# Kernel tuning notes

Hardware: AMD Instinct MI355X
Metric: run time of the kernel (lower is better)

The kernel has to match this reference:

```python
import jax, jax.numpy as jnp
import numpy as np

N_ATOMS = 100000
N_PAIRS = 3200000
F_ATOM, F_PAIR, H, F_OUT = 75, 14, 50, 50


def _linear_params(key, fan_in, fan_out):
    # torch.nn.Linear default init: U(-1/sqrt(fan_in), 1/sqrt(fan_in))
    kw, kb = jax.random.split(key)
    bound = 1.0 / np.sqrt(fan_in)
    W = jax.random.uniform(kw, (fan_out, fan_in), jnp.float32, -bound, bound)
    b = jax.random.uniform(kb, (fan_out,), jnp.float32, -bound, bound)
    return W, b


def setup_inputs() -> dict:
    key = jax.random.key(0)
    ks = jax.random.split(key, 12)
    atom_features = jax.random.normal(ks[0], (N_ATOMS, F_ATOM), jnp.float32)
    pair_features = jax.random.normal(ks[1], (N_PAIRS, F_PAIR), jnp.float32)
    pair_split = jnp.sort(jax.random.randint(ks[2], (N_PAIRS,), 0, N_ATOMS, jnp.int32))
    atom_to_pair = jax.random.randint(ks[3], (N_PAIRS, 2), 0, N_ATOMS, jnp.int32)
    W_AA, b_AA = _linear_params(ks[4], F_ATOM, H)
    W_PA, b_PA = _linear_params(ks[5], F_PAIR, H)
    W_A, b_A = _linear_params(ks[6], 2 * H, F_OUT)
    W_AP, b_AP = _linear_params(ks[7], 2 * F_ATOM, H)
    W_PP, b_PP = _linear_params(ks[8], F_PAIR, H)
    W_P, b_P = _linear_params(ks[9], 2 * H, F_OUT)
    return dict(atom_features=atom_features, pair_features=pair_features,
                pair_split=pair_split, atom_to_pair=atom_to_pair,
                W_AA=W_AA, b_AA=b_AA, W_PA=W_PA, b_PA=b_PA,
                W_A=W_A, b_A=b_A, W_AP=W_AP, b_AP=b_AP,
                W_PP=W_PP, b_PP=b_PP, W_P=W_P, b_P=b_P)


def reference(atom_features, pair_features, pair_split, atom_to_pair,
              W_AA, b_AA, W_PA, b_PA, W_A, b_A,
              W_AP, b_AP, W_PP, b_PP, W_P, b_P):
    relu = jax.nn.relu
    # atom update
    AA = relu(atom_features @ W_AA.T + b_AA)                      # [N_atoms, H]
    PA = relu(pair_features @ W_PA.T + b_PA)                      # [N_pairs, H]
    PA = jax.ops.segment_sum(PA, pair_split, num_segments=N_ATOMS)  # [N_atoms, H]
    A = relu(jnp.concatenate([AA, PA], axis=1) @ W_A.T + b_A)     # [N_atoms, F_OUT]
    # pair update
    pair_ij = atom_features[atom_to_pair].reshape(-1, 2 * F_ATOM)             # [N_pairs, 2F]
    pair_ji = atom_features[atom_to_pair[:, ::-1]].reshape(-1, 2 * F_ATOM)    # flipped order
    AP_ij = relu(pair_ij @ W_AP.T + b_AP)
    AP_ji = relu(pair_ji @ W_AP.T + b_AP)
    PP = relu(pair_features @ W_PP.T + b_PP)
    P = relu(jnp.concatenate([AP_ij + AP_ji, PP], axis=1) @ W_P.T + b_P)      # [N_pairs, F_OUT]
    return A, P
```

## Files before the change

kernel.cpp:

```cpp
#include <hip/hip_runtime.h>

#define NATOMS 100000
#define NPAIRS 3200000

using short8  = __attribute__((ext_vector_type(8))) short;
using float4v = __attribute__((ext_vector_type(4))) float;
using fx2     = __attribute__((ext_vector_type(2))) float;

__device__ __forceinline__ unsigned short f2bf(float f) {
    unsigned int u = __float_as_uint(f);
    unsigned int r = (u + 0x7fffu + ((u >> 16) & 1u)) >> 16;
    return (unsigned short)r;
}
__device__ __forceinline__ float bflo(unsigned int u) { return __uint_as_float(u << 16); }
__device__ __forceinline__ float bfhi(unsigned int u) { return __uint_as_float(u & 0xffff0000u); }
__device__ __forceinline__ unsigned int cvtpk(float lo, float hi) {
    unsigned int r;
    asm("v_cvt_pk_bf16_f32 %0, %1, %2" : "=v"(r) : "v"(lo), "v"(hi));
    return r;
}

__device__ __forceinline__ unsigned int fp8e(float v) {
    unsigned int u = __float_as_uint(v);
    unsigned int a = u & 0x7fffffffu;
    unsigned int r = a + 0x7FFFFu + ((a >> 20) & 1u);
    int e8 = (int)(r >> 23) - 120;
    unsigned int b = (e8 >= 1) ? (((unsigned int)e8 << 3) | ((r >> 20) & 7u)) : 0u;
    return b | ((u >> 24) & 0x80u);
}

#if __has_builtin(__builtin_amdgcn_cvt_pk_fp8_f32)
__device__ __forceinline__ unsigned int enc4(float a, float b, float c, float d) {
    int w = __builtin_amdgcn_cvt_pk_fp8_f32(a, b, 0, false);
    w = __builtin_amdgcn_cvt_pk_fp8_f32(c, d, w, true);
    return (unsigned int)w;
}
__device__ __forceinline__ unsigned short enc2(float a, float b) {
    return (unsigned short)(__builtin_amdgcn_cvt_pk_fp8_f32(a, b, 0, false) & 0xffff);
}
#else
__device__ __forceinline__ unsigned int enc4(float a, float b, float c, float d) {
    return fp8e(a) | (fp8e(b) << 8) | (fp8e(c) << 16) | (fp8e(d) << 24);
}
__device__ __forceinline__ unsigned short enc2(float a, float b) {
    return (unsigned short)(fp8e(a) | (fp8e(b) << 8));
}
#endif

#if __has_builtin(__builtin_amdgcn_cvt_pk_f32_fp8)
__device__ __forceinline__ fx2 dec8lo(unsigned int u) { return __builtin_amdgcn_cvt_pk_f32_fp8((int)u, false); }
__device__ __forceinline__ fx2 dec8hi(unsigned int u) { return __builtin_amdgcn_cvt_pk_f32_fp8((int)u, true); }
#else
__device__ __forceinline__ float fp8d_(unsigned int u, int sh) {
    unsigned int b = (u >> sh) & 0xffu;
    return __uint_as_float((((b & 0x7fu) << 20) + 0x3C000000u) | ((b & 0x80u) << 24));
}
__device__ __forceinline__ fx2 dec8lo(unsigned int u) { fx2 r; r.x = fp8d_(u, 0);  r.y = fp8d_(u, 8);  return r; }
__device__ __forceinline__ fx2 dec8hi(unsigned int u) { fx2 r; r.x = fp8d_(u, 16); r.y = fp8d_(u, 24); return r; }
#endif


__global__ __launch_bounds__(256) void k_wconv(
    const float* __restrict__ W_P,  const float* __restrict__ b_P,
    const float* __restrict__ W_PP, const float* __restrict__ b_PP,
    const float* __restrict__ W_PA, const float* __restrict__ b_PA,
    const float* __restrict__ W_AA, const float* __restrict__ b_AA,
    const float* __restrict__ W_AP, const float* __restrict__ b_AP,
    const float* __restrict__ W_A,  const float* __restrict__ b_A,
    unsigned short* __restrict__ WPb,  unsigned short* __restrict__ WPPb,
    unsigned short* __restrict__ WPAb, unsigned short* __restrict__ WATb,
    unsigned short* __restrict__ WAb,  float* __restrict__ PAsum)
{
    const int idx = blockIdx.x * 256 + threadIdx.x;
    if (idx < 64 * 128) {
        const int n = idx >> 7, k = idx & 127;
        float v = 0.0f, va = 0.0f;
        if (n < 50) {
            if (k < 50)                  { v = W_P[n * 100 + k];            va = W_A[n * 100 + k]; }
            else if (k == 50)            { v = b_P[n];                      va = b_A[n]; }
            else if (k >= 52 && k < 102) { v = W_P[n * 100 + 50 + (k - 52)]; va = W_A[n * 100 + 50 + (k - 52)]; }
        }
        WPb[idx] = f2bf(v);
        WAb[idx] = f2bf(va);
    }
    if (idx < 64 * 32) {
        const int n = idx >> 5, k = idx & 31;
        float vp = 0.0f, va = 0.0f;
        if (n < 50) {
            if (k < 14)      { vp = W_PP[n * 14 + k]; va = W_PA[n * 14 + k]; }
            else if (k == 14){ vp = b_PP[n];          va = b_PA[n]; }
        }
        WPPb[idx] = f2bf(vp);
        WPAb[idx] = f2bf(va);
    }
    if (idx < 160 * 96) {
        const int n = idx / 96, k = idx - n * 96;
        float v = 0.0f;
        if (n < 50) {
            if (k < 75)       v = W_AA[n * 75 + k];
            else if (k == 75) v = b_AA[n];
        } else if (n >= 52 && n < 102) {
            if (k < 75)       v = W_AP[(n - 52) * 150 + k];
            else if (k == 75) v = b_AP[n - 52];
        } else if (n >= 104 && n < 154) {
            if (k < 75)       v = W_AP[(n - 104) * 150 + 75 + k];
        }
        WATb[idx] = f2bf(v);
    }
    for (int i = idx; i < NATOMS * 50; i += 256 * 256) PAsum[i] = 0.0f;
}

__global__ __launch_bounds__(512) void k_atom_pre(
    const float* __restrict__ af,
    const unsigned short* __restrict__ WATb,
    unsigned short* __restrict__ AAb,
    unsigned short* __restrict__ XAu16)
{
    __shared__ unsigned short U16[128 * 128];

    const int t   = threadIdx.x;
    const int blk = blockIdx.x;
    const int pl  = t >> 2;
    const int sub = t & 3;
    const int w   = t >> 6;
    const int l   = t & 63;
    const int lr  = l & 15;
    const int lk  = l >> 4;
    const int a0  = blk * 128;

    {
        const int a = a0 + pl;
        const int swz = (pl & 7) << 2;
        unsigned int* urow = (unsigned int*)U16 + pl * 64;
        if (a < NATOMS) {
            const float* ar = af + (size_t)a * 75;
            if (sub < 3) {
                const int c0 = sub * 20;
#pragma unroll
                for (int q = 0; q < 10; ++q)
                    urow[(c0 / 2 + q) ^ swz] = cvtpk(ar[c0 + 2 * q], ar[c0 + 2 * q + 1]);
            } else {
#pragma unroll
                for (int q = 0; q < 7; ++q)
                    urow[(30 + q) ^ swz] = cvtpk(ar[60 + 2 * q], ar[60 + 2 * q + 1]);
                urow[37 ^ swz] = cvtpk(ar[74], 1.0f);
            }
        } else {
            if (sub < 3) {
                const int c0 = sub * 20;
#pragma unroll
                for (int q = 0; q < 10; ++q) urow[(c0 / 2 + q) ^ swz] = 0u;
            } else {
#pragma unroll
                for (int q = 30; q <= 37; ++q) urow[q ^ swz] = 0u;
            }
        }
        if (sub == 3) {
#pragma unroll
            for (int q = 38; q < 48; ++q) urow[q ^ swz] = 0u;
        }
#pragma unroll
        for (int q = 48 + sub; q < 64; q += 4) urow[q ^ swz] = 0u;
    }

    {
        const int row  = 16 * w + lr;
        const int aat  = a0 + row;
        const int swzb = (row & 7) << 4;
        const char* ub = (const char*)U16 + row * 256;
        short8 bf0 = *(const short8*)(ub + ((0   + lk * 16) ^ swzb));
        short8 bf1 = *(const short8*)(ub + ((64  + lk * 16) ^ swzb));
        short8 bf2 = *(const short8*)(ub + ((128 + lk * 16) ^ swzb));

#pragma unroll
        for (int nt = 0; nt < 10; ++nt) {
            float4v acc = {0.f, 0.f, 0.f, 0.f};
            const unsigned short* wr = WATb + (nt * 16 + lr) * 96 + lk * 8;
            acc = __builtin_amdgcn_mfma_f32_16x16x32_bf16(*(const short8*)(wr),      bf0, acc, 0, 0, 0);
            acc = __builtin_amdgcn_mfma_f32_16x16x32_bf16(*(const short8*)(wr + 32), bf1, acc, 0, 0, 0);
            acc = __builtin_amdgcn_mfma_f32_16x16x32_bf16(*(const short8*)(wr + 64), bf2, acc, 0, 0, 0);
            const int n0 = nt * 16 + lk * 4;
            if (aat < NATOMS) {
                if (n0 <= 48) {
                    if (n0 < 48) {
                        uint2 v;
                        v.x = cvtpk(fmaxf(acc[0], 0.f), fmaxf(acc[1], 0.f));
                        v.y = cvtpk(fmaxf(acc[2], 0.f), fmaxf(acc[3], 0.f));
                        *(uint2*)(AAb + (size_t)aat * 64 + n0) = v;
                    } else {
                        *(unsigned int*)(AAb + (size_t)aat * 64 + 48) =
                            cvtpk(fmaxf(acc[0], 0.f), fmaxf(acc[1], 0.f));
                    }
                } else if (n0 >= 52 && n0 <= 100) {
                    char* xb = (char*)XAu16 + (size_t)aat * 128;
                    if (n0 < 100) *(unsigned int*)(xb + (n0 - 52)) = enc4(acc[0], acc[1], acc[2], acc[3]);
                    else          *(unsigned short*)(xb + 48)      = enc2(acc[0], acc[1]);
                } else if (n0 >= 104 && n0 <= 152) {
                    char* xb = (char*)XAu16 + (size_t)aat * 128 + 64;
                    if (n0 < 152) *(unsigned int*)(xb + (n0 - 104)) = enc4(acc[0], acc[1], acc[2], acc[3]);
                    else          *(unsigned short*)(xb + 48)       = enc2(acc[0], acc[1]);
                }
            }
        }
    }
}

__device__ __forceinline__ void s_pair_u32(unsigned int x1i, unsigned int x2j,
    unsigned int x1j, unsigned int x2i, unsigned int* srow, int slot, int swz)
{
    fx2 aL = dec8lo(x1i), bL = dec8lo(x2j), cL = dec8lo(x1j), dL = dec8lo(x2i);
    fx2 aH = dec8hi(x1i), bH = dec8hi(x2j), cH = dec8hi(x1j), dH = dec8hi(x2i);
    float sL0 = fmaxf(aL.x + bL.x, 0.f) + fmaxf(cL.x + dL.x, 0.f);
    float sL1 = fmaxf(aL.y + bL.y, 0.f) + fmaxf(cL.y + dL.y, 0.f);
    float sH0 = fmaxf(aH.x + bH.x, 0.f) + fmaxf(cH.x + dH.x, 0.f);
    float sH1 = fmaxf(aH.y + bH.y, 0.f) + fmaxf(cH.y + dH.y, 0.f);
    srow[(slot)     ^ swz] = cvtpk(sL0, sL1);
    srow[(slot + 1) ^ swz] = cvtpk(sH0, sH1);
}
__device__ __forceinline__ void s_chunk16(uint4 X1i, uint4 X2j, uint4 X1j, uint4 X2i,
                                          int c, unsigned int* srow, int swz)
{
    const int o = 8 * c;
    s_pair_u32(X1i.x, X2j.x, X1j.x, X2i.x, srow, o + 0, swz);
    s_pair_u32(X1i.y, X2j.y, X1j.y, X2i.y, srow, o + 2, swz);
    s_pair_u32(X1i.z, X2j.z, X1j.z, X2i.z, srow, o + 4, swz);
    s_pair_u32(X1i.w, X2j.w, X1j.w, X2i.w, srow, o + 6, swz);
}

__global__ __launch_bounds__(512) void k_pair(
    const float* __restrict__ pf,
    const int* __restrict__ psplit,
    const int* __restrict__ a2p,
    const unsigned short* __restrict__ WPb,
    const unsigned short* __restrict__ WPPb,
    const unsigned short* __restrict__ WPAb,
    const unsigned short* __restrict__ XAu16,
    float* __restrict__ PAsum,
    float* __restrict__ Pout)
{
    __shared__ unsigned int  S32[128 * 64];
    __shared__ unsigned short U16[128 * 64];
    __shared__ int ps_lds[128];
    __shared__ unsigned char head_list[128];
    __shared__ int nheads;

    const int t   = threadIdx.x;
    const int blk = blockIdx.x;
    const int pl  = t >> 2;
    const int sub = t & 3;
    const int p   = blk * 128 + pl;
    const int w   = t >> 6;
    const int l   = t & 63;
    const int lr  = l & 15;
    const int lk  = l >> 4;

    if (t == 0) nheads = 0;
    if (t < 128) ps_lds[t] = psplit[blk * 128 + t];

    const int2 ij = ((const int2*)a2p)[p];
    float2 pfa, pfb, pfc, pfd;
    {
        const float2* pr2 = (const float2*)(pf + (size_t)p * 14);
        if (sub == 0) { pfa = pr2[0]; pfb = pr2[1]; pfc = pr2[2]; pfd = pr2[3]; }
        else if (sub == 1) { pfa = pr2[4]; pfb = pr2[5]; pfc = pr2[6]; }
    }

    const uint4* xi4 = (const uint4*)(XAu16 + (size_t)ij.x * 64);
    const uint4* xj4 = (const uint4*)(XAu16 + (size_t)ij.y * 64);
    uint4 X1i, X1j, X2i, X2j;
    unsigned int t12i = 0, t12j = 0, t28i = 0, t28j = 0;
    if (sub < 3) {
        X1i = xi4[sub];     X1j = xj4[sub];
        X2i = xi4[4 + sub]; X2j = xj4[4 + sub];
    } else {
        const unsigned int* xiu = (const unsigned int*)xi4;
        const unsigned int* xju = (const unsigned int*)xj4;
        t12i = xiu[12]; t12j = xju[12];
        t28i = xiu[28]; t28j = xju[28];
    }

    {
        uint4 q = {0u, 0u, 0u, 0u};
        if (sub == 0) {
            q.x = cvtpk(pfa.x, pfa.y); q.y = cvtpk(pfb.x, pfb.y);
            q.z = cvtpk(pfc.x, pfc.y); q.w = cvtpk(pfd.x, pfd.y);
        } else if (sub == 1) {
            q.x = cvtpk(pfa.x, pfa.y); q.y = cvtpk(pfb.x, pfb.y);
            q.z = cvtpk(pfc.x, pfc.y); q.w = 0x00003F80u;
        }
        *(uint4*)((char*)U16 + pl * 128 + ((16 * sub) ^ ((pl & 7) << 4))) = q;
    }

    {
        unsigned int* srow = &S32[pl * 64];
        const int swz = (pl & 7) << 2;
        if (sub < 3) {
            s_chunk16(X1i, X2j, X1j, X2i, sub, srow, swz);
        } else {
            fx2 aL = dec8lo(t12i), bL = dec8lo(t28j), cL = dec8lo(t12j), dL = dec8lo(t28i);
            float s48 = fmaxf(aL.x + bL.x, 0.f) + fmaxf(cL.x + dL.x, 0.f);
            float s49 = fmaxf(aL.y + bL.y, 0.f) + fmaxf(cL.y + dL.y, 0.f);
            srow[24 ^ swz] = cvtpk(s48, s49);
            srow[25 ^ swz] = 0x00003F80u;
#pragma unroll
            for (int u = 51; u <= 63; ++u) srow[u ^ swz] = 0u;
        }
    }

    {
        const int row  = 16 * w + lr;
        const int swz4 = (row & 7) << 2;
        const short8 bfrag = *(const short8*)((const char*)U16 + row * 128 + ((16 * lk) ^ ((row & 7) << 4)));
        unsigned int* srow = &S32[row * 64];
        unsigned int* U32  = (unsigned int*)U16;

#pragma unroll
        for (int nt = 0; nt < 4; ++nt) {
            short8 afr = *(const short8*)(WPPb + (nt * 16 + lr) * 32 + lk * 8);
            float4v acc = __builtin_amdgcn_mfma_f32_16x16x32_bf16(
                afr, bfrag, (float4v){0.f, 0.f, 0.f, 0.f}, 0, 0, 0);
            const int n0 = nt * 16 + lk * 4;
            if (n0 < 48) {
                uint2 v;
                v.x = cvtpk(fmaxf(acc[0], 0.f), fmaxf(acc[1], 0.f));
                v.y = cvtpk(fmaxf(acc[2], 0.f), fmaxf(acc[3], 0.f));
                *(uint2*)&srow[(26 + (n0 >> 1)) ^ swz4] = v;
            } else if (lk == 0) {
                srow[50 ^ swz4] = cvtpk(fmaxf(acc[0], 0.f), fmaxf(acc[1], 0.f));
            }
        }
#pragma unroll
        for (int nt = 0; nt < 4; ++nt) {
            short8 afr = *(const short8*)(WPAb + (nt * 16 + lr) * 32 + lk * 8);
            float4v acc = __builtin_amdgcn_mfma_f32_16x16x32_bf16(
                afr, bfrag, (float4v){0.f, 0.f, 0.f, 0.f}, 0, 0, 0);
            const int n0 = nt * 16 + lk * 4;
            if (n0 < 48) {
                uint2 v;
                v.x = cvtpk(fmaxf(acc[0], 0.f), fmaxf(acc[1], 0.f));
                v.y = cvtpk(fmaxf(acc[2], 0.f), fmaxf(acc[3], 0.f));
                *(uint2*)&U32[row * 32 + (((n0 >> 1)) ^ swz4)] = v;
            } else if (lk == 0) {
                U32[row * 32 + (24 ^ swz4)] = cvtpk(fmaxf(acc[0], 0.f), fmaxf(acc[1], 0.f));
            }
        }
    }

    {
        const int row = 16 * w + lr;
        short8 sfrag[4];
        const char* srowb = (const char*)&S32[row * 64];
#pragma unroll
        for (int ks = 0; ks < 4; ++ks)
            sfrag[ks] = *(const short8*)(srowb + ((64 * ks + 16 * lk) ^ ((row & 7) << 4)));
        float* po = Pout + ((size_t)blk * 128 + row) * 50;
#pragma unroll
        for (int nt = 0; nt < 4; ++nt) {
            float4v acc = {0.f, 0.f, 0.f, 0.f};
#pragma unroll
            for (int ks = 0; ks < 4; ++ks) {
                short8 wf = *(const short8*)(WPb + (nt * 16 + lr) * 128 + ks * 32 + lk * 8);
                acc = __builtin_amdgcn_mfma_f32_16x16x32_bf16(wf, sfrag[ks], acc, 0, 0, 0);
            }
            const int n0 = nt * 16 + lk * 4;
            if (n0 < 48) {
                float2 v0 = {fmaxf(acc[0], 0.f), fmaxf(acc[1], 0.f)};
                float2 v1 = {fmaxf(acc[2], 0.f), fmaxf(acc[3], 0.f)};
                *(float2*)(po + n0)     = v0;
                *(float2*)(po + n0 + 2) = v1;
            } else if (lk == 0) {
                float2 v0 = {fmaxf(acc[0], 0.f), fmaxf(acc[1], 0.f)};
                *(float2*)(po + 48) = v0;
            }
        }
    }

    __syncthreads();
    if (t < 128) {
        bool head = ((t & 31) == 0) || (ps_lds[t] != ps_lds[t - 1]);
        if (head) {
            int idx = atomicAdd(&nheads, 1);
            head_list[idx] = (unsigned char)t;
        }
    }
    __syncthreads();

    const int nh = nheads;
    const unsigned int* U32c = (const unsigned int*)U16;
    for (int iw = t; iw < nh * 25; iw += 512) {
        const int r0  = head_list[iw / 25];
        const int jc  = iw % 25;
        const int seg = ps_lds[r0];
        float a0 = 0.0f, a1 = 0.0f;
        int rr = r0;
        do {
            unsigned int u = U32c[rr * 32 + (jc ^ ((rr & 7) << 2))];
            a0 += bflo(u);
            a1 += bfhi(u);
            ++rr;
        } while (rr < 128 && (rr & 31) != 0 && ps_lds[rr] == seg);
        atomicAdd(&PAsum[(size_t)seg * 50 + 2 * jc],     a0);
        atomicAdd(&PAsum[(size_t)seg * 50 + 2 * jc + 1], a1);
    }
}

__global__ __launch_bounds__(512) void k_atom_final(
    const unsigned short* __restrict__ AAb,
    const float* __restrict__ PAsum,
    const unsigned short* __restrict__ WAb,
    float* __restrict__ Aout)
{
    __shared__ unsigned short U16[128 * 128];

    const int t   = threadIdx.x;
    const int blk = blockIdx.x;
    const int pl  = t >> 2;
    const int sub = t & 3;
    const int w   = t >> 6;
    const int l   = t & 63;
    const int lr  = l & 15;
    const int lk  = l >> 4;
    const int a0  = blk * 128;

    {
        const int a = a0 + pl;
        const int swz = (pl & 7) << 2;
        unsigned int* urow = (unsigned int*)U16 + pl * 64;
        if (a < NATOMS) {
            const unsigned int* aab = (const unsigned int*)AAb + (size_t)a * 32;
            if (sub < 3) {
#pragma unroll
                for (int q = 0; q < 7; ++q) urow[(7 * sub + q) ^ swz] = aab[7 * sub + q];
            } else {
#pragma unroll
                for (int q = 21; q < 25; ++q) urow[q ^ swz] = aab[q];
                urow[25 ^ swz] = 0x00003F80u;
            }
            const float* ps = PAsum + (size_t)a * 50;
            const int c0 = 14 * sub;
            const int np = (sub < 3) ? 7 : 4;
#pragma unroll
            for (int q = 0; q < 7; ++q) {
                if (q < np)
                    urow[(26 + c0 / 2 + q) ^ swz] = cvtpk(ps[c0 + 2 * q], ps[c0 + 2 * q + 1]);
            }
        } else {
            if (sub < 3) {
#pragma unroll
                for (int q = 0; q < 7; ++q) { urow[(7 * sub + q) ^ swz] = 0u; urow[(26 + 7 * sub + q) ^ swz] = 0u; }
            } else {
#pragma unroll
                for (int q = 21; q < 26; ++q) urow[q ^ swz] = 0u;
#pragma unroll
                for (int q = 47; q < 51; ++q) urow[q ^ swz] = 0u;
            }
        }
#pragma unroll
        for (int q = 51 + sub; q < 64; q += 4) urow[q ^ swz] = 0u;
    }

    {
        const int row  = 16 * w + lr;
        const int aat  = a0 + row;
        const int swzb = (row & 7) << 4;
        const char* ub = (const char*)U16 + row * 256;
        short8 bf[4];
#pragma unroll
        for (int ks = 0; ks < 4; ++ks)
            bf[ks] = *(const short8*)(ub + ((ks * 64 + lk * 16) ^ swzb));

        float* ao = Aout + (size_t)aat * 50;
#pragma unroll
        for (int nt = 0; nt < 4; ++nt) {
            float4v acc = {0.f, 0.f, 0.f, 0.f};
#pragma unroll
            for (int ks = 0; ks < 4; ++ks) {
                short8 wf = *(const short8*)(WAb + (nt * 16 + lr) * 128 + ks * 32 + lk * 8);
                acc = __builtin_amdgcn_mfma_f32_16x16x32_bf16(wf, bf[ks], acc, 0, 0, 0);
            }
            const int n0 = nt * 16 + lk * 4;
            if (aat < NATOMS) {
                if (n0 < 48) {
                    float2 v0 = {fmaxf(acc[0], 0.f), fmaxf(acc[1], 0.f)};
                    float2 v1 = {fmaxf(acc[2], 0.f), fmaxf(acc[3], 0.f)};
                    *(float2*)(ao + n0)     = v0;
                    *(float2*)(ao + n0 + 2) = v1;
                } else if (lk == 0 && nt == 3) {
                    float2 v0 = {fmaxf(acc[0], 0.f), fmaxf(acc[1], 0.f)};
                    *(float2*)(ao + 48) = v0;
                }
            }
        }
    }
}

extern "C" void kernel_launch(void* const* d_in, const int* in_sizes, int n_in,
                              void* d_out, int out_size, void* d_ws, size_t ws_size,
                              hipStream_t stream)
{
    const float* atom_features = (const float*)d_in[0];
    const float* pair_features = (const float*)d_in[1];
    const int*   pair_split    = (const int*)d_in[2];
    const int*   atom_to_pair  = (const int*)d_in[3];
    const float* W_AA = (const float*)d_in[4];
    const float* b_AA = (const float*)d_in[5];
    const float* W_PA = (const float*)d_in[6];
    const float* b_PA = (const float*)d_in[7];
    const float* W_A  = (const float*)d_in[8];
    const float* b_A  = (const float*)d_in[9];
    const float* W_AP = (const float*)d_in[10];
    const float* b_AP = (const float*)d_in[11];
    const float* W_PP = (const float*)d_in[12];
    const float* b_PP = (const float*)d_in[13];
    const float* W_P  = (const float*)d_in[14];
    const float* b_P  = (const float*)d_in[15];

    float* out   = (float*)d_out;
    float* A_out = out;
    float* P_out = out + (size_t)NATOMS * 50;

    unsigned short* AAb   = (unsigned short*)d_ws;
    unsigned short* XAu16 = AAb + (size_t)NATOMS * 64;
    float*          PAsum = (float*)(XAu16 + (size_t)NATOMS * 64);
    unsigned short* WPb   = (unsigned short*)(PAsum + (size_t)NATOMS * 50);
    unsigned short* WPPb  = WPb + 64 * 128;
    unsigned short* WPAb  = WPPb + 64 * 32;
    unsigned short* WATb  = WPAb + 64 * 32;
    unsigned short* WAb   = WATb + 160 * 96;

    k_wconv<<<256, 256, 0, stream>>>(W_P, b_P, W_PP, b_PP, W_PA, b_PA,
                                     W_AA, b_AA, W_AP, b_AP, W_A, b_A,
                                     WPb, WPPb, WPAb, WATb, WAb, PAsum);

    k_atom_pre<<<(NATOMS + 127) / 128, 512, 0, stream>>>(
        atom_features, WATb, AAb, XAu16);

    k_pair<<<NPAIRS / 128, 512, 0, stream>>>(
        pair_features, pair_split, atom_to_pair,
        WPb, WPPb, WPAb, XAu16, PAsum, P_out);

    k_atom_final<<<(NATOMS + 127) / 128, 512, 0, stream>>>(
        AAb, PAsum, WAb, A_out);
}
```

Measured before the change: 691.1 us.

## Drop U16 LDS buffer: bpermute pair fragment, pack PA into S32 padding as fp8

Removes the separate U16 shared buffer in k_pair. The pair-feature MFMA B-fragment is now built with ds_bpermute across lanes instead of a round trip through LDS, and the per-pair PA activations are stored as fp8 in the unused padding columns 51-63 of the S32 rows. Segment reduction now uses 8-row chunks with 4 features per work item. This cuts LDS footprint (raising occupancy) and LDS traffic, but PA now passes through fp8 (lower precision) and the shorter chunks may issue more global atomics.

```diff
diff --git a/kernel.cpp b/kernel.cpp
--- a/kernel.cpp
+++ b/kernel.cpp
@@ -35,15 +35,15 @@
     w = __builtin_amdgcn_cvt_pk_fp8_f32(c, d, w, true);
     return (unsigned int)w;
 }
-__device__ __forceinline__ unsigned short enc2(float a, float b) {
-    return (unsigned short)(__builtin_amdgcn_cvt_pk_fp8_f32(a, b, 0, false) & 0xffff);
+__device__ __forceinline__ unsigned int enc2(float a, float b) {
+    return (unsigned int)(__builtin_amdgcn_cvt_pk_fp8_f32(a, b, 0, false) & 0xffff);
 }
 #else
 __device__ __forceinline__ unsigned int enc4(float a, float b, float c, float d) {
     return fp8e(a) | (fp8e(b) << 8) | (fp8e(c) << 16) | (fp8e(d) << 24);
 }
-__device__ __forceinline__ unsigned short enc2(float a, float b) {
-    return (unsigned short)(fp8e(a) | (fp8e(b) << 8));
+__device__ __forceinline__ unsigned int enc2(float a, float b) {
+    return fp8e(a) | (fp8e(b) << 8);
 }
 #endif
 
@@ -76,8 +76,8 @@
         const int n = idx >> 7, k = idx & 127;
         float v = 0.0f, va = 0.0f;
         if (n < 50) {
-            if (k < 50)                  { v = W_P[n * 100 + k];            va = W_A[n * 100 + k]; }
-            else if (k == 50)            { v = b_P[n];                      va = b_A[n]; }
+            if (k < 50)                  { v = W_P[n * 100 + k];             va = W_A[n * 100 + k]; }
+            else if (k == 50)            { v = b_P[n];                       va = b_A[n]; }
             else if (k >= 52 && k < 102) { v = W_P[n * 100 + 50 + (k - 52)]; va = W_A[n * 100 + 50 + (k - 52)]; }
         }
         WPb[idx] = f2bf(v);
@@ -194,11 +194,11 @@
                 } else if (n0 >= 52 && n0 <= 100) {
                     char* xb = (char*)XAu16 + (size_t)aat * 128;
                     if (n0 < 100) *(unsigned int*)(xb + (n0 - 52)) = enc4(acc[0], acc[1], acc[2], acc[3]);
-                    else          *(unsigned short*)(xb + 48)      = enc2(acc[0], acc[1]);
+                    else          *(unsigned short*)(xb + 48)      = (unsigned short)enc2(acc[0], acc[1]);
                 } else if (n0 >= 104 && n0 <= 152) {
                     char* xb = (char*)XAu16 + (size_t)aat * 128 + 64;
                     if (n0 < 152) *(unsigned int*)(xb + (n0 - 104)) = enc4(acc[0], acc[1], acc[2], acc[3]);
-                    else          *(unsigned short*)(xb + 48)       = enc2(acc[0], acc[1]);
+                    else          *(unsigned short*)(xb + 48)       = (unsigned short)enc2(acc[0], acc[1]);
                 }
             }
         }
@@ -238,8 +238,7 @@
     float* __restrict__ PAsum,
     float* __restrict__ Pout)
 {
-    __shared__ unsigned int  S32[128 * 64];
-    __shared__ unsigned short U16[128 * 64];
+    __shared__ unsigned int S32[128 * 64];
     __shared__ int ps_lds[128];
     __shared__ unsigned char head_list[128];
     __shared__ int nheads;
@@ -279,16 +278,13 @@
         t28i = xiu[28]; t28j = xju[28];
     }
 
-    {
-        uint4 q = {0u, 0u, 0u, 0u};
-        if (sub == 0) {
-            q.x = cvtpk(pfa.x, pfa.y); q.y = cvtpk(pfb.x, pfb.y);
-            q.z = cvtpk(pfc.x, pfc.y); q.w = cvtpk(pfd.x, pfd.y);
-        } else if (sub == 1) {
-            q.x = cvtpk(pfa.x, pfa.y); q.y = cvtpk(pfb.x, pfb.y);
-            q.z = cvtpk(pfc.x, pfc.y); q.w = 0x00003F80u;
-        }
-        *(uint4*)((char*)U16 + pl * 128 + ((16 * sub) ^ ((pl & 7) << 4))) = q;
+    uint4 q = {0u, 0u, 0u, 0u};
+    if (sub == 0) {
+        q.x = cvtpk(pfa.x, pfa.y); q.y = cvtpk(pfb.x, pfb.y);
+        q.z = cvtpk(pfc.x, pfc.y); q.w = cvtpk(pfd.x, pfd.y);
+    } else if (sub == 1) {
+        q.x = cvtpk(pfa.x, pfa.y); q.y = cvtpk(pfb.x, pfb.y);
+        q.z = cvtpk(pfc.x, pfc.y); q.w = 0x00003F80u;
     }
 
     {
@@ -302,17 +298,20 @@
             float s49 = fmaxf(aL.y + bL.y, 0.f) + fmaxf(cL.y + dL.y, 0.f);
             srow[24 ^ swz] = cvtpk(s48, s49);
             srow[25 ^ swz] = 0x00003F80u;
-#pragma unroll
-            for (int u = 51; u <= 63; ++u) srow[u ^ swz] = 0u;
         }
     }
 
     {
         const int row  = 16 * w + lr;
         const int swz4 = (row & 7) << 2;
-        const short8 bfrag = *(const short8*)((const char*)U16 + row * 128 + ((16 * lk) ^ ((row & 7) << 4)));
+        const int src  = (4 * lr + lk) << 2;
+        uint4 bv;
+        bv.x = (unsigned int)__builtin_amdgcn_ds_bpermute(src, (int)q.x);
+        bv.y = (unsigned int)__builtin_amdgcn_ds_bpermute(src, (int)q.y);
+        bv.z = (unsigned int)__builtin_amdgcn_ds_bpermute(src, (int)q.z);
+        bv.w = (unsigned int)__builtin_amdgcn_ds_bpermute(src, (int)q.w);
+        const short8 bfrag = *(const short8*)&bv;
         unsigned int* srow = &S32[row * 64];
-        unsigned int* U32  = (unsigned int*)U16;
 
 #pragma unroll
         for (int nt = 0; nt < 4; ++nt) {
@@ -335,13 +334,12 @@
             float4v acc = __builtin_amdgcn_mfma_f32_16x16x32_bf16(
                 afr, bfrag, (float4v){0.f, 0.f, 0.f, 0.f}, 0, 0, 0);
             const int n0 = nt * 16 + lk * 4;
+            float r0 = fmaxf(acc[0], 0.f), r1 = fmaxf(acc[1], 0.f);
+            float r2 = fmaxf(acc[2], 0.f), r3 = fmaxf(acc[3], 0.f);
             if (n0 < 48) {
-                uint2 v;
-                v.x = cvtpk(fmaxf(acc[0], 0.f), fmaxf(acc[1], 0.f));
-                v.y = cvtpk(fmaxf(acc[2], 0.f), fmaxf(acc[3], 0.f));
-                *(uint2*)&U32[row * 32 + (((n0 >> 1)) ^ swz4)] = v;
+                srow[(51 + (n0 >> 2)) ^ swz4] = enc4(r0, r1, r2, r3);
             } else if (lk == 0) {
-                U32[row * 32 + (24 ^ swz4)] = cvtpk(fmaxf(acc[0], 0.f), fmaxf(acc[1], 0.f));
+                srow[63 ^ swz4] = enc2(r0, r1);
             }
         }
     }
@@ -377,7 +375,7 @@
 
     __syncthreads();
     if (t < 128) {
-        bool head = ((t & 31) == 0) || (ps_lds[t] != ps_lds[t - 1]);
+        bool head = ((t & 7) == 0) || (ps_lds[t] != ps_lds[t - 1]);
         if (head) {
             int idx = atomicAdd(&nheads, 1);
             head_list[idx] = (unsigned char)t;
@@ -386,21 +384,25 @@
     __syncthreads();
 
     const int nh = nheads;
-    const unsigned int* U32c = (const unsigned int*)U16;
-    for (int iw = t; iw < nh * 25; iw += 512) {
-        const int r0  = head_list[iw / 25];
-        const int jc  = iw % 25;
+    for (int iw = t; iw < nh * 13; iw += 512) {
+        const int r0  = head_list[iw / 13];
+        const int c   = iw % 13;
         const int seg = ps_lds[r0];
-        float a0 = 0.0f, a1 = 0.0f;
+        float a0 = 0.f, a1 = 0.f, a2 = 0.f, a3 = 0.f;
         int rr = r0;
         do {
-            unsigned int u = U32c[rr * 32 + (jc ^ ((rr & 7) << 2))];
-            a0 += bflo(u);
-            a1 += bfhi(u);
+            unsigned int u = S32[rr * 64 + ((51 + c) ^ ((rr & 7) << 2))];
+            fx2 lo = dec8lo(u), hi = dec8hi(u);
+            a0 += lo.x; a1 += lo.y; a2 += hi.x; a3 += hi.y;
             ++rr;
-        } while (rr < 128 && (rr & 31) != 0 && ps_lds[rr] == seg);
-        atomicAdd(&PAsum[(size_t)seg * 50 + 2 * jc],     a0);
-        atomicAdd(&PAsum[(size_t)seg * 50 + 2 * jc + 1], a1);
+        } while (rr < 128 && (rr & 7) != 0 && ps_lds[rr] == seg);
+        const int f = 4 * c;
+        atomicAdd(&PAsum[(size_t)seg * 50 + f],     a0);
+        atomicAdd(&PAsum[(size_t)seg * 50 + f + 1], a1);
+        if (f + 2 < 50) {
+            atomicAdd(&PAsum[(size_t)seg * 50 + f + 2], a2);
+            atomicAdd(&PAsum[(size_t)seg * 50 + f + 3], a3);
+        }
     }
 }
 
```

After: 1.100 ms. 1.59x slower.
